# Performance work log

Measured on AMD Instinct MI355X. Metric: run time of the kernel, lower is better.

The kernel has to match this reference:

```python
import jax, jax.numpy as jnp
import numpy as np

EPS = 1e-6
H = 8          # num_heads
GAMMA = 0.99   # fixed decay (requires_grad=False in source)
RPE_LAYERS = 3


def srms(x):
    # SimpleRMSNorm: x / (rms(x) + eps), rms = ||x||_2 / sqrt(d) = sqrt(mean(x^2))
    return x / (jnp.sqrt(jnp.mean(x * x, axis=-1, keepdims=True)) + EPS)


def setup_inputs() -> dict:
    key = jax.random.key(0)
    B, N, E = 8, 2048, 512
    D1 = 1536            # int(3*512) // 8 * 8
    R = 512              # rpe_embedding
    ks = jax.random.split(key, 12)

    def lin(k, i, o):
        return jax.random.normal(k, (i, o), jnp.float32) * (i ** -0.5)

    x = jax.random.normal(ks[0], (B, N, E), jnp.float32)
    return {
        "x": x,
        "Wu": lin(ks[1], E, D1), "bu": jnp.zeros((D1,), jnp.float32),
        "Wv": lin(ks[2], E, D1), "bv": jnp.zeros((D1,), jnp.float32),
        "Wo": lin(ks[3], D1, E), "bo": jnp.zeros((E,), jnp.float32),
        "rpe_Win": lin(ks[4], 1, R), "rpe_bin": jnp.zeros((R,), jnp.float32),
        "rpe_W": jax.random.normal(ks[5], (RPE_LAYERS, R, R), jnp.float32) * (R ** -0.5),
        "rpe_b": jnp.zeros((RPE_LAYERS, R), jnp.float32),
        "rpe_Wout": lin(ks[6], R, D1), "rpe_bout": jnp.zeros((D1,), jnp.float32),
    }


def reference(x, Wu, bu, Wv, bv, Wo, bo, rpe_Win, rpe_bin, rpe_W, rpe_b, rpe_Wout, rpe_bout):
    B, N, E = x.shape
    u = jax.nn.silu(x @ Wu + bu)                     # b n d1
    v = jax.nn.silu(x @ Wv + bv)                     # b n d1
    D1 = v.shape[-1]
    D = D1 // H
    v = v.reshape(B, N, H, D).transpose(0, 2, 1, 3)  # b h n d

    # RPE MLP over positions: row 0 is the zero index, rows 1..N-1 are pos indices 1..N-1 (par_type=1)
    idx = jnp.arange(0, N, dtype=x.dtype)[:, None]   # (N, 1)
    h = idx @ rpe_Win + rpe_bin                      # (N, R)
    for i in range(RPE_LAYERS):                      # residual=False
        h = jax.nn.relu(srms(h)) @ rpe_W[i] + rpe_b[i]
    coeffs = jax.nn.relu(srms(h)) @ rpe_Wout + rpe_bout   # (N, H*D)
    coeffs = coeffs.reshape(N, H, D).transpose(1, 0, 2)   # h n d

    zero = coeffs[:, :1]                             # h 1 d  (a_0)
    pos = coeffs[:, 1:]                              # h n-1 d (a_1..a_{n-1})
    decay = GAMMA ** jnp.arange(1, N, dtype=x.dtype)[None, :, None]
    pos = pos * decay
    # causal: a = [a0, a1..a_{n-1}, a0]; act_type='none' -> identity
    a = jnp.concatenate([zero, pos, zero], axis=1)   # h, n+1, d

    # Toeplitz mixing via circular convolution of length 2n (torch.fft.rfft/irfft, norm='backward')
    m = 2 * N
    yf = jnp.fft.rfft(v, m, axis=2)                  # b h m/2+1 d (complex)
    af = jnp.fft.rfft(a, m, axis=1)[None]            # 1 h m/2+1 d
    out = jnp.fft.irfft(yf * af, m, axis=2)[:, :, :N, :]  # b h n d

    out = out.transpose(0, 2, 1, 3).reshape(B, N, D1)     # b n (h d)
    out = u * out
    return out @ Wo + bo
```

## Files before the change

### kernel.cpp

```cpp
#include <hip/hip_runtime.h>
#include <cstdint>


typedef unsigned short ushort_t;
typedef __attribute__((ext_vector_type(8))) short short8;
typedef __attribute__((ext_vector_type(4))) float f32x4;

#define AS1 __attribute__((address_space(1)))
#define AS3 __attribute__((address_space(3)))

#define SW1(j) ((j) ^ (((j) >> 4) & 15))
#define SW2(j) ((j) ^ ((((j) >> 6) & 7) << 1))

__device__ __forceinline__ int xcd_swz(int bid, int nwg) {
  return (bid & 7) * (nwg >> 3) + (bid >> 3);
}

__device__ __forceinline__ float bf2f(ushort_t b) {
  union { unsigned u; float f; } x; x.u = ((unsigned)b) << 16; return x.f;
}
__device__ __forceinline__ ushort_t f2bf(float f) {
  union { float f; unsigned u; } x; x.f = f;
  unsigned r = x.u + 0x7fffu + ((x.u >> 16) & 1u);
  return (ushort_t)(r >> 16);
}

__device__ __forceinline__ void gload_lds16(const void* g, void* l) {
  auto gp = reinterpret_cast<const AS1 unsigned*>(reinterpret_cast<uintptr_t>(g));
  auto lp = reinterpret_cast<AS3 unsigned*>(reinterpret_cast<uintptr_t>(l));
  __builtin_amdgcn_global_load_lds(gp, lp, 16, 0, 0);
}

template<int MODE>
__launch_bounds__(256, 2)
__global__ void gemm_bt(const ushort_t* __restrict__ A, const ushort_t* __restrict__ Bt,
                        const float* __restrict__ bias, void* __restrict__ Cout,
                        void* __restrict__ Cout2, int M, int N, int K, float lng)
{
  __shared__ ushort_t As[128 * 64];
  __shared__ ushort_t Bs[128 * 64];
  const int tid  = threadIdx.x;
  const int wave = tid >> 6, lane = tid & 63;
  const int nb = N >> 7;
  const int lbid = xcd_swz((int)blockIdx.x, (int)gridDim.x);
  const int bm = lbid / nb, bn = lbid % nb;
  const int m0 = bm << 7, n0 = bn << 7;
  const int lrow = lane & 15, quad = lane >> 4;
  const int wm = (wave >> 1) << 6, wn = (wave & 1) << 6;
  const int srow = lane >> 3;
  const int scol = (lane & 7) << 3;

  f32x4 acc[4][4] = {};

  for (int kt = 0; kt < K; kt += 64) {
    __syncthreads();
#pragma unroll
    for (int i = 0; i < 4; ++i) {
      const int ci  = i * 4 + wave;
      const int row = ci * 8 + srow;
      gload_lds16(A  + (long)(m0 + row) * K + kt + scol, (void*)&As[ci * 512]);
      gload_lds16(Bt + (long)(n0 + row) * K + kt + scol, (void*)&Bs[ci * 512]);
    }
    __syncthreads();
#pragma unroll
    for (int s = 0; s < 2; ++s) {
      short8 afr[4], bfr[4];
#pragma unroll
      for (int i = 0; i < 4; ++i)
        afr[i] = *(const short8*)&As[(wm + i * 16 + lrow) * 64 + s * 32 + quad * 8];
#pragma unroll
      for (int j = 0; j < 4; ++j)
        bfr[j] = *(const short8*)&Bs[(wn + j * 16 + lrow) * 64 + s * 32 + quad * 8];
#pragma unroll
      for (int i = 0; i < 4; ++i)
#pragma unroll
        for (int j = 0; j < 4; ++j)
          acc[i][j] = __builtin_amdgcn_mfma_f32_16x16x32_bf16(afr[i], bfr[j], acc[i][j], 0, 0, 0);
    }
  }

#pragma unroll
  for (int i = 0; i < 4; ++i) {
    const int rowb = m0 + wm + i * 16 + quad * 4;
#pragma unroll
    for (int j = 0; j < 4; ++j) {
      const int col = n0 + wn + j * 16 + lrow;
      const float bv = bias[col];
      if (MODE == 0) {
#pragma unroll
        for (int r = 0; r < 4; ++r)
          ((float*)Cout)[(long)(rowb + r) * N + col] = acc[i][j][r] + bv;
      } else {
        if (col < 1536) {
#pragma unroll
          for (int r = 0; r < 4; ++r) {
            float val = acc[i][j][r] + bv;
            float sv = val / (1.f + __expf(-val));
            ((ushort_t*)Cout)[(long)(rowb + r) * 1536 + col] = f2bf(sv);
          }
        } else {
          union { ushort_t h[4]; uint2 u2; } pk;
#pragma unroll
          for (int r = 0; r < 4; ++r) {
            float val = acc[i][j][r] + bv;
            float sv = val / (1.f + __expf(-val));
            pk.h[r] = f2bf(sv);
          }
          *(uint2*)((ushort_t*)Cout2 + (long)(col - 1536) * 16384 + rowb) = pk.u2;
        }
      }
    }
  }
}

template<int MODE>
__launch_bounds__(256, 2)
__global__ void gemm64_bt(const ushort_t* __restrict__ A, const float* __restrict__ Af,
                          const ushort_t* __restrict__ Bt,
                          const float* __restrict__ bias, float* __restrict__ Cout,
                          int M, int N, int K, float lng)
{
  constexpr bool NORM = (MODE >= 4);
  __shared__ ushort_t As[64 * 64];
  __shared__ ushort_t Bs[64 * 64];
  __shared__ float rsc[64];
  const int tid = threadIdx.x, wave = tid >> 6, lane = tid & 63;
  const int nb = N >> 6;
  const int lbid = xcd_swz((int)blockIdx.x, (int)gridDim.x);
  const int bm = lbid / nb, bn = lbid % nb;
  const int m0 = bm << 6, n0 = bn << 6;
  const int lrow = lane & 15, quad = lane >> 4;
  const int wm = (wave >> 1) << 5, wn = (wave & 1) << 5;
  const int srow = lane >> 3, scol = (lane & 7) << 3;

  if (NORM) {
    const int prow = tid >> 2, pq = tid & 3;
    const float* hr = Af + (long)(m0 + prow) * 512 + pq * 128;
    float ss = 0.f;
#pragma unroll 8
    for (int c = 0; c < 128; c += 4) {
      float4 f = *(const float4*)(hr + c);
      ss += f.x * f.x + f.y * f.y + f.z * f.z + f.w * f.w;
    }
    ss += __shfl_xor(ss, 1);
    ss += __shfl_xor(ss, 2);
    if (pq == 0) rsc[prow] = 1.f / (sqrtf(ss * (1.f / 512.f)) + 1e-6f);
  }

  f32x4 acc[2][2] = {};

  for (int kt = 0; kt < K; kt += 64) {
    __syncthreads();
#pragma unroll
    for (int i = 0; i < 2; ++i) {
      const int ci = i * 4 + wave;
      const int row = ci * 8 + srow;
      if (!NORM) {
        gload_lds16(A + (long)(m0 + row) * K + kt + scol, (void*)&As[ci * 512]);
      } else {
        const float* hp = Af + (long)(m0 + row) * 512 + kt + scol;
        float4 f0 = *(const float4*)hp;
        float4 f1 = *(const float4*)(hp + 4);
        const float sc = rsc[row];
        unsigned p0 = (unsigned)f2bf(fmaxf(f0.x * sc, 0.f)) |
                      ((unsigned)f2bf(fmaxf(f0.y * sc, 0.f)) << 16);
        unsigned p1 = (unsigned)f2bf(fmaxf(f0.z * sc, 0.f)) |
                      ((unsigned)f2bf(fmaxf(f0.w * sc, 0.f)) << 16);
        unsigned p2 = (unsigned)f2bf(fmaxf(f1.x * sc, 0.f)) |
                      ((unsigned)f2bf(fmaxf(f1.y * sc, 0.f)) << 16);
        unsigned p3 = (unsigned)f2bf(fmaxf(f1.z * sc, 0.f)) |
                      ((unsigned)f2bf(fmaxf(f1.w * sc, 0.f)) << 16);
        *(uint4*)&As[ci * 512 + srow * 64 + scol] = make_uint4(p0, p1, p2, p3);
      }
      gload_lds16(Bt + (long)(n0 + row) * K + kt + scol, (void*)&Bs[ci * 512]);
    }
    __syncthreads();
#pragma unroll
    for (int s = 0; s < 2; ++s) {
      short8 afr[2], bfr[2];
#pragma unroll
      for (int i = 0; i < 2; ++i)
        afr[i] = *(const short8*)&As[(wm + i * 16 + lrow) * 64 + s * 32 + quad * 8];
#pragma unroll
      for (int j = 0; j < 2; ++j)
        bfr[j] = *(const short8*)&Bs[(wn + j * 16 + lrow) * 64 + s * 32 + quad * 8];
#pragma unroll
      for (int i = 0; i < 2; ++i)
#pragma unroll
        for (int j = 0; j < 2; ++j)
          acc[i][j] = __builtin_amdgcn_mfma_f32_16x16x32_bf16(afr[i], bfr[j], acc[i][j], 0, 0, 0);
    }
  }

#pragma unroll
  for (int i = 0; i < 2; ++i) {
    const int rowb = m0 + wm + i * 16 + quad * 4;
#pragma unroll
    for (int j = 0; j < 2; ++j) {
      const int col = n0 + wn + j * 16 + lrow;
      const float bv = bias[col];
#pragma unroll
      for (int r = 0; r < 4; ++r) {
        const int row = rowb + r;
        float val = acc[i][j][r] + bv;
        if (MODE == 0 || MODE == 4) Cout[(long)row * N + col] = val;
        else                        Cout[(long)col * M + row] = val * __expf(lng * (float)row);
      }
    }
  }
}

__device__ __forceinline__ void srms_relu_store(float v0, float v1, ushort_t* out,
                                                long rowbase, int tid)
{
  float ss = v0 * v0 + v1 * v1;
#pragma unroll
  for (int off = 32; off; off >>= 1) ss += __shfl_down(ss, off);
  __shared__ float ps[4];
  const int wave = tid >> 6, lane = tid & 63;
  if (lane == 0) ps[wave] = ss;
  __syncthreads();
  float tot = ps[0] + ps[1] + ps[2] + ps[3];
  float sc = 1.f / (sqrtf(tot * (1.f / 512.f)) + 1e-6f);
  out[rowbase + tid]       = f2bf(fmaxf(v0 * sc, 0.f));
  out[rowbase + tid + 256] = f2bf(fmaxf(v1 * sc, 0.f));
}

__device__ __forceinline__ void wtrans_body(const float* __restrict__ src,
                                            ushort_t* __restrict__ dst,
                                            int K, int N, int lb, int tid,
                                            float (*tile)[33])
{
  const int nbx = N >> 5;
  const int bx = lb % nbx, by = lb / nbx;
  const int n0 = bx << 5, k0 = by << 5;
  const int tx = tid & 31, ty = tid >> 5;
  for (int yy = ty; yy < 32; yy += 8)
    tile[yy][tx] = src[(long)(k0 + yy) * N + n0 + tx];
  __syncthreads();
  for (int yy = ty; yy < 32; yy += 8)
    dst[(long)(n0 + yy) * K + k0 + tx] = f2bf(tile[tx][yy]);
}

__launch_bounds__(256)
__global__ void prep_all(const float* __restrict__ Wu, const float* __restrict__ Wv,
                         const float* __restrict__ Wo, const float* __restrict__ rW,
                         const float* __restrict__ rWout,
                         const float* __restrict__ bu, const float* __restrict__ bv,
                         const float* __restrict__ x,
                         const float* __restrict__ rWin, const float* __restrict__ rbin,
                         ushort_t* __restrict__ wuvt, ushort_t* __restrict__ wot,
                         ushort_t* __restrict__ wrt, ushort_t* __restrict__ wroutt,
                         float* __restrict__ buvb, ushort_t* __restrict__ xb,
                         float2* __restrict__ twg, float2* __restrict__ twh,
                         ushort_t* __restrict__ a0)
{
  __shared__ float tile[32][33];
  const int bid = blockIdx.x, tid = threadIdx.x;
  if (bid < 3840) {
    const float* src; ushort_t* dst; int K, N, lb;
    if (bid < 768)       { src = Wu;    dst = wuvt;              K = 512;  N = 1536; lb = bid; }
    else if (bid < 1536) { src = Wv;    dst = wuvt + 1536L*512;  K = 512;  N = 1536; lb = bid - 768; }
    else if (bid < 2304) { src = Wo;    dst = wot;               K = 1536; N = 512;  lb = bid - 1536; }
    else if (bid < 2560) { src = rW;              dst = wrt;              K = 512; N = 512; lb = bid - 2304; }
    else if (bid < 2816) { src = rW + 512L*512;   dst = wrt + 512L*512;   K = 512; N = 512; lb = bid - 2560; }
    else if (bid < 3072) { src = rW + 2L*512*512; dst = wrt + 2L*512*512; K = 512; N = 512; lb = bid - 2816; }
    else                 { src = rWout; dst = wroutt;            K = 512;  N = 1536; lb = bid - 3072; }
    wtrans_body(src, dst, K, N, lb, tid, tile);
  } else if (bid < 3846) {
    int i = (bid - 3840) * 256 + tid;
    if (i < 1536) { buvb[i] = bu[i]; buvb[1536 + i] = bv[i]; }
  } else if (bid < 12038) {
    long i = (long)(bid - 3846) * 1024 + tid * 4;
    float4 f = *(const float4*)(x + i);
    unsigned lo = (unsigned)f2bf(f.x) | ((unsigned)f2bf(f.y) << 16);
    unsigned hi = (unsigned)f2bf(f.z) | ((unsigned)f2bf(f.w) << 16);
    *(uint2*)(xb + i) = make_uint2(lo, hi);
  } else if (bid < 12046) {
    int j = (bid - 12038) * 256 + tid;
    float s, c;
    __sincosf((float)j * (6.283185307179586f / 2048.f), &s, &c);
    twg[j] = make_float2(c, -s);
    float s2, c2;
    __sincosf((float)j * (3.14159265358979f / 2048.f), &s2, &c2);
    twh[j] = make_float2(c2, -s2);
  } else {
    const int n = bid - 12046;
    const float fn = (float)n;
    float v0 = fn * rWin[tid] + rbin[tid];
    float v1 = fn * rWin[tid + 256] + rbin[tid + 256];
    srms_relu_store(v0, v1, a0, (long)n * 512, tid);
  }
}

__device__ __forceinline__ float2 cmulf(float2 a, float2 b) {
  return make_float2(a.x * b.x - a.y * b.y, a.x * b.y + a.y * b.x);
}
__device__ __forceinline__ float4 c2add(float4 p, float4 q){
  return make_float4(p.x+q.x, p.y+q.y, p.z+q.z, p.w+q.w);
}
__device__ __forceinline__ float4 c2sub(float4 p, float4 q){
  return make_float4(p.x-q.x, p.y-q.y, p.z-q.z, p.w-q.w);
}
__device__ __forceinline__ float4 c2mni(float4 z){
  return make_float4(z.y, -z.x, z.w, -z.z);
}
__device__ __forceinline__ float4 c2w8(float4 z){
  const float s = 0.70710678118654752f;
  return make_float4(s*(z.x+z.y), s*(z.y-z.x), s*(z.z+z.w), s*(z.w-z.z));
}
__device__ __forceinline__ float4 c2w83(float4 z){
  const float s = 0.70710678118654752f;
  return make_float4(s*(z.y-z.x), -s*(z.x+z.y), s*(z.w-z.z), -s*(z.z+z.w));
}
__device__ __forceinline__ float4 c2mul(float4 z, float2 w){
  return make_float4(z.x*w.x - z.y*w.y, z.x*w.y + z.y*w.x,
                     z.z*w.x - z.w*w.y, z.z*w.y + z.w*w.x);
}

__device__ __forceinline__ void dft8d(const float4* u, float4* y)
{
  float4 a0=c2add(u[0],u[4]), a1=c2add(u[1],u[5]), a2=c2add(u[2],u[6]), a3=c2add(u[3],u[7]);
  float4 b0=c2sub(u[0],u[4]), b1=c2w8(c2sub(u[1],u[5])), b2=c2mni(c2sub(u[2],u[6])), b3=c2w83(c2sub(u[3],u[7]));
  float4 c0=c2add(a0,a2), c1=c2sub(a0,a2), c2=c2add(a1,a3), c3=c2mni(c2sub(a1,a3));
  y[0]=c2add(c0,c2); y[2]=c2add(c1,c3); y[4]=c2sub(c0,c2); y[6]=c2sub(c1,c3);
  float4 d0=c2add(b0,b2), d1=c2sub(b0,b2), d2=c2add(b1,b3), d3=c2mni(c2sub(b1,b3));
  y[1]=c2add(d0,d2); y[3]=c2add(d1,d3); y[5]=c2sub(d0,d2); y[7]=c2sub(d1,d3);
}
__device__ __forceinline__ void dft8d_hz(const float4* u, float4* y)
{
  float4 b1=c2w8(u[1]), b2=c2mni(u[2]), b3=c2w83(u[3]);
  float4 c0=c2add(u[0],u[2]), c1=c2sub(u[0],u[2]), c2=c2add(u[1],u[3]), c3=c2mni(c2sub(u[1],u[3]));
  y[0]=c2add(c0,c2); y[2]=c2add(c1,c3); y[4]=c2sub(c0,c2); y[6]=c2sub(c1,c3);
  float4 d0=c2add(u[0],b2), d1=c2sub(u[0],b2), d2=c2add(b1,b3), d3=c2mni(c2sub(b1,b3));
  y[1]=c2add(d0,d2); y[3]=c2add(d1,d3); y[5]=c2sub(d0,d2); y[7]=c2sub(d1,d3);
}

template<bool HZ>
__device__ void fft2048_ip4(float4* b, const float2* __restrict__ tw, int tid)
{
  float4 u[8], y[8];
  {
    const int i = tid;
#pragma unroll
    for (int m = 0; m < (HZ ? 4 : 8); ++m) u[m] = b[i + 256*m];
    if (HZ) dft8d_hz(u, y); else dft8d(u, y);
    __syncthreads();
    const int j = i << 3;
#pragma unroll
    for (int m = 0; m < 8; ++m) b[SW1(j + m)] = y[m];
  }
  __syncthreads();
  {
    const int i = tid, k = i & 7, tb = k << 5;
    float2 w[8];
#pragma unroll
    for (int m = 1; m < 8; ++m) w[m] = tw[m * tb];
#pragma unroll
    for (int m = 0; m < 8; ++m) u[m] = b[SW1(i + 256*m)];
#pragma unroll
    for (int m = 1; m < 8; ++m) u[m] = c2mul(u[m], w[m]);
    dft8d(u, y);
    __syncthreads();
    const int j = ((i - k) << 3) + k;
#pragma unroll
    for (int m = 0; m < 8; ++m) b[SW2(j + 8*m)] = y[m];
  }
  __syncthreads();
  {
    const int i = tid, k = i & 63, tb = k << 2;
    float2 w[8];
#pragma unroll
    for (int m = 1; m < 8; ++m) w[m] = tw[m * tb];
#pragma unroll
    for (int m = 0; m < 8; ++m) u[m] = b[SW2(i + 256*m)];
#pragma unroll
    for (int m = 1; m < 8; ++m) u[m] = c2mul(u[m], w[m]);
    dft8d(u, y);
    __syncthreads();
    const int j = ((i - k) << 3) + k;
#pragma unroll
    for (int m = 0; m < 8; ++m) b[j + 64*m] = y[m];
  }
  __syncthreads();
#pragma unroll
  for (int hh = 0; hh < 2; ++hh) {
    const int i = tid + (hh << 8);
    float2 w1 = tw[i], w2 = tw[2 * i], w3 = tw[3 * i];
    float4 q0 = b[i], q1 = b[i + 512], q2 = b[i + 1024], q3 = b[i + 1536];
    q1 = c2mul(q1, w1); q2 = c2mul(q2, w2); q3 = c2mul(q3, w3);
    float4 v0 = c2add(q0, q2), v2 = c2sub(q0, q2);
    float4 v1 = c2add(q1, q3), v3 = c2mni(c2sub(q1, q3));
    b[i]        = c2add(v0, v1);
    b[i + 512]  = c2add(v2, v3);
    b[i + 1024] = c2sub(v0, v1);
    b[i + 1536] = c2sub(v2, v3);
  }
  __syncthreads();
}

__launch_bounds__(256, 4)
__global__ void fft_kernel_spec(const float* __restrict__ kern, float2* __restrict__ af,
                                const float2* __restrict__ twg, const float2* __restrict__ twh)
{
  __shared__ float4 bx[2048];
  const int tid = threadIdx.x;
  const int c0 = (int)blockIdx.x * 2;
  const float* ka = kern + (long)c0 * 2048;
  const float* kb = ka + 2048;
  for (int j = tid; j < 1024; j += 256) {
    float2 A = *(const float2*)(ka + 2 * j);
    float2 B = *(const float2*)(kb + 2 * j);
    bx[j] = make_float4(A.x, A.y, B.x, B.y);
  }
  __syncthreads();
  fft2048_ip4<true>(bx, twg, tid);
  float2* af0 = af + (long)c0 * 2052;
  float2* af1 = af0 + 2052;
  for (int k = tid; k <= 1024; k += 256) {
    const float2 W = twh[k];
    const int kn = (2048 - k) & 2047;
    const float4 Zk4 = bx[k], Zn4 = bx[kn];
    {
      float2 Zk = make_float2(Zk4.x, Zk4.y), Zn = make_float2(Zn4.x, Zn4.y);
      float2 E = make_float2(0.5f * (Zk.x + Zn.x), 0.5f * (Zk.y - Zn.y));
      float2 O = make_float2(0.5f * (Zk.y + Zn.y), 0.5f * (Zn.x - Zk.x));
      float2 WO = cmulf(W, O);
      af0[k] = make_float2(E.x + WO.x, E.y + WO.y);
      if (k != 0 && k != 1024) af0[2048 - k] = make_float2(E.x - WO.x, -(E.y - WO.y));
      if (k == 0)              af0[2048]     = make_float2(E.x - WO.x, -(E.y - WO.y));
    }
    {
      float2 Zk = make_float2(Zk4.z, Zk4.w), Zn = make_float2(Zn4.z, Zn4.w);
      float2 E = make_float2(0.5f * (Zk.x + Zn.x), 0.5f * (Zk.y - Zn.y));
      float2 O = make_float2(0.5f * (Zk.y + Zn.y), 0.5f * (Zn.x - Zk.x));
      float2 WO = cmulf(W, O);
      af1[k] = make_float2(E.x + WO.x, E.y + WO.y);
      if (k != 0 && k != 1024) af1[2048 - k] = make_float2(E.x - WO.x, -(E.y - WO.y));
      if (k == 0)              af1[2048]     = make_float2(E.x - WO.x, -(E.y - WO.y));
    }
  }
}

__launch_bounds__(256, 4)
__global__ void fft_conv(ushort_t* __restrict__ vt, const float2* __restrict__ af,
                         const float2* __restrict__ twg, const float2* __restrict__ twh)
{
  __shared__ float4 bx[2048];
  const int tid = threadIdx.x;
  const long s0 = (long)blockIdx.x * 2;
  const int c = (int)(s0 >> 3);
  ushort_t* vsa = vt + s0 * 2048;
  ushort_t* vsb = vsa + 2048;
#pragma unroll
  for (int jj = 0; jj < 4; ++jj) {
    const int j = tid + jj * 256;
    unsigned pa = *(const unsigned*)(vsa + 2 * j);
    unsigned pb = *(const unsigned*)(vsb + 2 * j);
    bx[j] = make_float4(bf2f((ushort_t)(pa & 0xffffu)), bf2f((ushort_t)(pa >> 16)),
                        bf2f((ushort_t)(pb & 0xffffu)), bf2f((ushort_t)(pb >> 16)));
  }
  __syncthreads();
  fft2048_ip4<true>(bx, twg, tid);
  const float2* afc = af + (long)c * 2052;
  for (int k = tid; k <= 1024; k += 256) {
    const float2 A0 = afc[k], A1 = afc[2048 - k], W = twh[k];
    const float2 cW = make_float2(W.x, -W.y);
    const int kn = (2048 - k) & 2047;
    const float4 Zk4 = bx[k], Zn4 = bx[kn];
    float2 ya0, yn0, ya1, yn1;
    {
      float2 Zk = make_float2(Zk4.x, Zk4.y), Zn = make_float2(Zn4.x, Zn4.y);
      float2 E = make_float2(0.5f * (Zk.x + Zn.x), 0.5f * (Zk.y - Zn.y));
      float2 O = make_float2(0.5f * (Zk.y + Zn.y), 0.5f * (Zn.x - Zk.x));
      float2 WO = cmulf(W, O);
      float2 Xk = make_float2(E.x + WO.x, E.y + WO.y);
      float2 Xn = make_float2(E.x - WO.x, -(E.y - WO.y));
      float2 Pk = cmulf(Xk, A0);
      float2 Pn = cmulf(Xn, A1);
      float2 E2 = make_float2(0.5f * (Pk.x + Pn.x), 0.5f * (Pk.y - Pn.y));
      float2 G  = make_float2(0.5f * (Pk.x - Pn.x), 0.5f * (Pk.y + Pn.y));
      float2 Fo = cmulf(cW, G);
      ya0 = make_float2(E2.x - Fo.y, -(E2.y + Fo.x));
      yn0 = make_float2(E2.x + Fo.y, E2.y - Fo.x);
    }
    {
      float2 Zk = make_float2(Zk4.z, Zk4.w), Zn = make_float2(Zn4.z, Zn4.w);
      float2 E = make_float2(0.5f * (Zk.x + Zn.x), 0.5f * (Zk.y - Zn.y));
      float2 O = make_float2(0.5f * (Zk.y + Zn.y), 0.5f * (Zn.x - Zk.x));
      float2 WO = cmulf(W, O);
      float2 Xk = make_float2(E.x + WO.x, E.y + WO.y);
      float2 Xn = make_float2(E.x - WO.x, -(E.y - WO.y));
      float2 Pk = cmulf(Xk, A0);
      float2 Pn = cmulf(Xn, A1);
      float2 E2 = make_float2(0.5f * (Pk.x + Pn.x), 0.5f * (Pk.y - Pn.y));
      float2 G  = make_float2(0.5f * (Pk.x - Pn.x), 0.5f * (Pk.y + Pn.y));
      float2 Fo = cmulf(cW, G);
      ya1 = make_float2(E2.x - Fo.y, -(E2.y + Fo.x));
      yn1 = make_float2(E2.x + Fo.y, E2.y - Fo.x);
    }
    bx[k] = make_float4(ya0.x, ya0.y, ya1.x, ya1.y);
    if (k != 0 && k != 1024)
      bx[2048 - k] = make_float4(yn0.x, yn0.y, yn1.x, yn1.y);
  }
  __syncthreads();
  fft2048_ip4<false>(bx, twg, tid);
  const float inv = 1.f / 2048.f;
#pragma unroll
  for (int jj = 0; jj < 4; ++jj) {
    const int j = tid + jj * 256;
    float4 r = bx[j];
    unsigned oa = (unsigned)f2bf(r.x * inv) | ((unsigned)f2bf(-r.y * inv) << 16);
    unsigned ob = (unsigned)f2bf(r.z * inv) | ((unsigned)f2bf(-r.w * inv) << 16);
    *(unsigned*)(vsa + 2 * j) = oa;
    *(unsigned*)(vsb + 2 * j) = ob;
  }
}

__launch_bounds__(256)
__global__ void gate_trans(const ushort_t* __restrict__ convt, ushort_t* __restrict__ u)
{
  __shared__ ushort_t tile[64][65];
  const int bc = (int)blockIdx.x % 24, br = (int)blockIdx.x / 24;
  const int c0 = bc << 6, r0 = br << 6;
  const int tx = threadIdx.x & 63, ty = threadIdx.x >> 6;
  for (int yy = ty; yy < 64; yy += 4)
    tile[yy][tx] = convt[(long)(c0 + yy) * 16384 + r0 + tx];
  __syncthreads();
  for (int yy = ty; yy < 64; yy += 4) {
    long ui = (long)(r0 + yy) * 1536 + c0 + tx;
    float uu = bf2f(u[ui]);
    float cc = bf2f(tile[tx][yy]);
    u[ui] = f2bf(uu * cc);
  }
}

extern "C" void kernel_launch(void* const* d_in, const int* in_sizes, int n_in,
                              void* d_out, int out_size, void* d_ws, size_t ws_size,
                              hipStream_t stream)
{
  const float* x     = (const float*)d_in[0];
  const float* Wu    = (const float*)d_in[1];
  const float* bu    = (const float*)d_in[2];
  const float* Wv    = (const float*)d_in[3];
  const float* bv    = (const float*)d_in[4];
  const float* Wo    = (const float*)d_in[5];
  const float* bo    = (const float*)d_in[6];
  const float* rWin  = (const float*)d_in[7];
  const float* rbin  = (const float*)d_in[8];
  const float* rW    = (const float*)d_in[9];
  const float* rb    = (const float*)d_in[10];
  const float* rWout = (const float*)d_in[11];
  const float* rbout = (const float*)d_in[12];

  char* base = (char*)d_ws;
  size_t off = 0;
  auto alloc = [&](size_t bytes) -> char* {
    size_t r = (off + 255) & ~(size_t)255; off = r + bytes; return base + r;
  };
  ushort_t* wuvt   = (ushort_t*)alloc(3072L * 512 * 2);
  ushort_t* wot    = (ushort_t*)alloc(512L * 1536 * 2);
  ushort_t* wrt    = (ushort_t*)alloc(3L * 512 * 512 * 2);
  ushort_t* wroutt = (ushort_t*)alloc(1536L * 512 * 2);
  float*    buvb   = (float*)   alloc(3072L * 4);
  ushort_t* a0     = (ushort_t*)alloc(2048L * 512 * 2);
  float2*   af     = (float2*)  alloc(1536L * 2052 * 8);
  float2*   twg    = (float2*)  alloc(2048L * 8);
  float2*   twh    = (float2*)  alloc(2048L * 8);
  char*     X      = alloc(16384L * 512 * 2);
  ushort_t* u      = (ushort_t*)alloc(16384L * 1536 * 2);
  ushort_t* vt     = (ushort_t*)alloc(1536L * 16384 * 2);
  ushort_t* xb   = (ushort_t*)X;
  float*    hA   = (float*)X;
  float*    hB   = (float*)(X + 4L * 1024 * 1024);
  float*    kern = (float*)(X + 4L * 1024 * 1024);

  const float lng = -0.01005033585350145f;

  prep_all<<<dim3(14094), dim3(256), 0, stream>>>(
      Wu, Wv, Wo, rW, rWout, bu, bv, x, rWin, rbin,
      wuvt, wot, wrt, wroutt, buvb, xb, twg, twh, a0);

  gemm_bt<3><<<dim3(3072), dim3(256), 0, stream>>>(xb, wuvt, buvb, u, vt,
                                                   16384, 3072, 512, 0.f);

  gemm64_bt<0><<<dim3(256), dim3(256), 0, stream>>>(a0, nullptr, wrt,
                                                    rb, hA, 2048, 512, 512, 0.f);
  gemm64_bt<4><<<dim3(256), dim3(256), 0, stream>>>(nullptr, hA, wrt + 512L*512,
                                                    rb + 512, hB, 2048, 512, 512, 0.f);
  gemm64_bt<4><<<dim3(256), dim3(256), 0, stream>>>(nullptr, hB, wrt + 2L*512*512,
                                                    rb + 1024, hA, 2048, 512, 512, 0.f);
  gemm64_bt<5><<<dim3(768), dim3(256), 0, stream>>>(nullptr, hA, wroutt,
                                                    rbout, kern, 2048, 1536, 512, lng);
  fft_kernel_spec<<<dim3(768), dim3(256), 0, stream>>>(kern, af, twg, twh);

  fft_conv<<<dim3(6144), dim3(256), 0, stream>>>(vt, af, twg, twh);
  gate_trans<<<dim3(6144), dim3(256), 0, stream>>>(vt, u);
  gemm_bt<0><<<dim3(512), dim3(256), 0, stream>>>(u, wot, bo, d_out, nullptr,
                                                  16384, 512, 1536, 0.f);
}
```

Baseline: 459.7 us.

## Replace packed 2048-point real-FFT trick with full 4096-point complex FFT

The FFT convolution previously packed two real channels into one complex 2048-point transform, then split them with a half-length twiddle and post-processing step. It now runs a full 4096-point complex FFT with two real channels packed as real and imaginary parts. The kernel spectrum is stored at full length, and the inverse transform uses a conjugate trick. This removes the split/merge post-processing and one twiddle table. In exchange it roughly doubles the FFT work and LDS traffic per block and doubles the spectrum buffer size.

```diff
diff --git a/kernel.cpp b/kernel.cpp
--- a/kernel.cpp
+++ b/kernel.cpp
@@ -9,8 +9,8 @@
 #define AS1 __attribute__((address_space(1)))
 #define AS3 __attribute__((address_space(3)))
 
-#define SW1(j) ((j) ^ (((j) >> 4) & 15))
-#define SW2(j) ((j) ^ ((((j) >> 6) & 7) << 1))
+#define SWA(j) ((j) ^ (((j) >> 3) & 15))
+#define SWB(j) ((j) ^ ((((j) >> 6) & 7) << 1))
 
 __device__ __forceinline__ int xcd_swz(int bid, int nwg) {
   return (bid & 7) * (nwg >> 3) + (bid >> 3);
@@ -252,8 +252,7 @@
                          ushort_t* __restrict__ wuvt, ushort_t* __restrict__ wot,
                          ushort_t* __restrict__ wrt, ushort_t* __restrict__ wroutt,
                          float* __restrict__ buvb, ushort_t* __restrict__ xb,
-                         float2* __restrict__ twg, float2* __restrict__ twh,
-                         ushort_t* __restrict__ a0)
+                         float2* __restrict__ twf, ushort_t* __restrict__ a0)
 {
   __shared__ float tile[32][33];
   const int bid = blockIdx.x, tid = threadIdx.x;
@@ -276,16 +275,13 @@
     unsigned lo = (unsigned)f2bf(f.x) | ((unsigned)f2bf(f.y) << 16);
     unsigned hi = (unsigned)f2bf(f.z) | ((unsigned)f2bf(f.w) << 16);
     *(uint2*)(xb + i) = make_uint2(lo, hi);
-  } else if (bid < 12046) {
+  } else if (bid < 12054) {
     int j = (bid - 12038) * 256 + tid;
     float s, c;
-    __sincosf((float)j * (6.283185307179586f / 2048.f), &s, &c);
-    twg[j] = make_float2(c, -s);
-    float s2, c2;
-    __sincosf((float)j * (3.14159265358979f / 2048.f), &s2, &c2);
-    twh[j] = make_float2(c2, -s2);
+    __sincosf((float)j * (6.283185307179586f / 4096.f), &s, &c);
+    twf[j] = make_float2(c, -s);
   } else {
-    const int n = bid - 12046;
+    const int n = bid - 12054;
     const float fn = (float)n;
     float v0 = fn * rWin[tid] + rbin[tid];
     float v1 = fn * rWin[tid + 256] + rbin[tid + 256];
@@ -296,157 +292,159 @@
 __device__ __forceinline__ float2 cmulf(float2 a, float2 b) {
   return make_float2(a.x * b.x - a.y * b.y, a.x * b.y + a.y * b.x);
 }
-__device__ __forceinline__ float4 c2add(float4 p, float4 q){
-  return make_float4(p.x+q.x, p.y+q.y, p.z+q.z, p.w+q.w);
-}
-__device__ __forceinline__ float4 c2sub(float4 p, float4 q){
-  return make_float4(p.x-q.x, p.y-q.y, p.z-q.z, p.w-q.w);
-}
-__device__ __forceinline__ float4 c2mni(float4 z){
-  return make_float4(z.y, -z.x, z.w, -z.z);
-}
-__device__ __forceinline__ float4 c2w8(float4 z){
+__device__ __forceinline__ float2 cadds(float2 a, float2 b){ return make_float2(a.x+b.x, a.y+b.y); }
+__device__ __forceinline__ float2 csubs(float2 a, float2 b){ return make_float2(a.x-b.x, a.y-b.y); }
+__device__ __forceinline__ float2 cmnis(float2 z){ return make_float2(z.y, -z.x); }
+__device__ __forceinline__ float2 cw8s(float2 z){
   const float s = 0.70710678118654752f;
-  return make_float4(s*(z.x+z.y), s*(z.y-z.x), s*(z.z+z.w), s*(z.w-z.z));
-}
-__device__ __forceinline__ float4 c2w83(float4 z){
+  return make_float2(s*(z.x+z.y), s*(z.y-z.x));
+}
+__device__ __forceinline__ float2 cw83s(float2 z){
   const float s = 0.70710678118654752f;
-  return make_float4(s*(z.y-z.x), -s*(z.x+z.y), s*(z.w-z.z), -s*(z.z+z.w));
-}
-__device__ __forceinline__ float4 c2mul(float4 z, float2 w){
-  return make_float4(z.x*w.x - z.y*w.y, z.x*w.y + z.y*w.x,
-                     z.z*w.x - z.w*w.y, z.z*w.y + z.w*w.x);
-}
-
-__device__ __forceinline__ void dft8d(const float4* u, float4* y)
-{
-  float4 a0=c2add(u[0],u[4]), a1=c2add(u[1],u[5]), a2=c2add(u[2],u[6]), a3=c2add(u[3],u[7]);
-  float4 b0=c2sub(u[0],u[4]), b1=c2w8(c2sub(u[1],u[5])), b2=c2mni(c2sub(u[2],u[6])), b3=c2w83(c2sub(u[3],u[7]));
-  float4 c0=c2add(a0,a2), c1=c2sub(a0,a2), c2=c2add(a1,a3), c3=c2mni(c2sub(a1,a3));
-  y[0]=c2add(c0,c2); y[2]=c2add(c1,c3); y[4]=c2sub(c0,c2); y[6]=c2sub(c1,c3);
-  float4 d0=c2add(b0,b2), d1=c2sub(b0,b2), d2=c2add(b1,b3), d3=c2mni(c2sub(b1,b3));
-  y[1]=c2add(d0,d2); y[3]=c2add(d1,d3); y[5]=c2sub(d0,d2); y[7]=c2sub(d1,d3);
-}
-__device__ __forceinline__ void dft8d_hz(const float4* u, float4* y)
-{
-  float4 b1=c2w8(u[1]), b2=c2mni(u[2]), b3=c2w83(u[3]);
-  float4 c0=c2add(u[0],u[2]), c1=c2sub(u[0],u[2]), c2=c2add(u[1],u[3]), c3=c2mni(c2sub(u[1],u[3]));
-  y[0]=c2add(c0,c2); y[2]=c2add(c1,c3); y[4]=c2sub(c0,c2); y[6]=c2sub(c1,c3);
-  float4 d0=c2add(u[0],b2), d1=c2sub(u[0],b2), d2=c2add(b1,b3), d3=c2mni(c2sub(b1,b3));
-  y[1]=c2add(d0,d2); y[3]=c2add(d1,d3); y[5]=c2sub(d0,d2); y[7]=c2sub(d1,d3);
+  return make_float2(s*(z.y-z.x), -s*(z.x+z.y));
+}
+
+__device__ __forceinline__ void dft8s(const float2* u, float2* y)
+{
+  float2 a0=cadds(u[0],u[4]), a1=cadds(u[1],u[5]), a2=cadds(u[2],u[6]), a3=cadds(u[3],u[7]);
+  float2 b0=csubs(u[0],u[4]), b1=cw8s(csubs(u[1],u[5])), b2=cmnis(csubs(u[2],u[6])), b3=cw83s(csubs(u[3],u[7]));
+  float2 c0=cadds(a0,a2), c1=csubs(a0,a2), c2=cadds(a1,a3), c3=cmnis(csubs(a1,a3));
+  y[0]=cadds(c0,c2); y[2]=cadds(c1,c3); y[4]=csubs(c0,c2); y[6]=csubs(c1,c3);
+  float2 d0=cadds(b0,b2), d1=csubs(b0,b2), d2=cadds(b1,b3), d3=cmnis(csubs(b1,b3));
+  y[1]=cadds(d0,d2); y[3]=cadds(d1,d3); y[5]=csubs(d0,d2); y[7]=csubs(d1,d3);
+}
+__device__ __forceinline__ void dft8s_hz(const float2* u, float2* y)
+{
+  float2 b1=cw8s(u[1]), b2=cmnis(u[2]), b3=cw83s(u[3]);
+  float2 c0=cadds(u[0],u[2]), c1=csubs(u[0],u[2]), c2=cadds(u[1],u[3]), c3=cmnis(csubs(u[1],u[3]));
+  y[0]=cadds(c0,c2); y[2]=cadds(c1,c3); y[4]=csubs(c0,c2); y[6]=csubs(c1,c3);
+  float2 d0=cadds(u[0],b2), d1=csubs(u[0],b2), d2=cadds(b1,b3), d3=cmnis(csubs(b1,b3));
+  y[1]=cadds(d0,d2); y[3]=cadds(d1,d3); y[5]=csubs(d0,d2); y[7]=csubs(d1,d3);
 }
 
 template<bool HZ>
-__device__ void fft2048_ip4(float4* b, const float2* __restrict__ tw, int tid)
-{
-  float4 u[8], y[8];
-  {
-    const int i = tid;
-#pragma unroll
-    for (int m = 0; m < (HZ ? 4 : 8); ++m) u[m] = b[i + 256*m];
-    if (HZ) dft8d_hz(u, y); else dft8d(u, y);
-    __syncthreads();
-    const int j = i << 3;
-#pragma unroll
-    for (int m = 0; m < 8; ++m) b[SW1(j + m)] = y[m];
-  }
-  __syncthreads();
-  {
-    const int i = tid, k = i & 7, tb = k << 5;
-    float2 w[8];
-#pragma unroll
-    for (int m = 1; m < 8; ++m) w[m] = tw[m * tb];
-#pragma unroll
-    for (int m = 0; m < 8; ++m) u[m] = b[SW1(i + 256*m)];
-#pragma unroll
-    for (int m = 1; m < 8; ++m) u[m] = c2mul(u[m], w[m]);
-    dft8d(u, y);
-    __syncthreads();
-    const int j = ((i - k) << 3) + k;
-#pragma unroll
-    for (int m = 0; m < 8; ++m) b[SW2(j + 8*m)] = y[m];
-  }
-  __syncthreads();
-  {
-    const int i = tid, k = i & 63, tb = k << 2;
-    float2 w[8];
-#pragma unroll
-    for (int m = 1; m < 8; ++m) w[m] = tw[m * tb];
-#pragma unroll
-    for (int m = 0; m < 8; ++m) u[m] = b[SW2(i + 256*m)];
-#pragma unroll
-    for (int m = 1; m < 8; ++m) u[m] = c2mul(u[m], w[m]);
-    dft8d(u, y);
-    __syncthreads();
-    const int j = ((i - k) << 3) + k;
-#pragma unroll
-    for (int m = 0; m < 8; ++m) b[j + 64*m] = y[m];
-  }
-  __syncthreads();
-#pragma unroll
-  for (int hh = 0; hh < 2; ++hh) {
-    const int i = tid + (hh << 8);
-    float2 w1 = tw[i], w2 = tw[2 * i], w3 = tw[3 * i];
-    float4 q0 = b[i], q1 = b[i + 512], q2 = b[i + 1024], q3 = b[i + 1536];
-    q1 = c2mul(q1, w1); q2 = c2mul(q2, w2); q3 = c2mul(q3, w3);
-    float4 v0 = c2add(q0, q2), v2 = c2sub(q0, q2);
-    float4 v1 = c2add(q1, q3), v3 = c2mni(c2sub(q1, q3));
-    b[i]        = c2add(v0, v1);
-    b[i + 512]  = c2add(v2, v3);
-    b[i + 1024] = c2sub(v0, v1);
-    b[i + 1536] = c2sub(v2, v3);
-  }
-  __syncthreads();
+__device__ __forceinline__ void f4k_s1(float2* b, int tid)
+{
+  float2 u[8], u2[8], y[8], y2[8];
+#pragma unroll
+  for (int m = 0; m < (HZ ? 4 : 8); ++m) {
+    u[m]  = b[tid + 512*m];
+    u2[m] = b[tid + 256 + 512*m];
+  }
+  if (HZ) { dft8s_hz(u, y); dft8s_hz(u2, y2); }
+  else    { dft8s(u, y);    dft8s(u2, y2); }
+  __syncthreads();
+  const int j1 = tid << 3;
+#pragma unroll
+  for (int m = 0; m < 8; ++m) {
+    b[SWA(j1 + m)]        = y[m];
+    b[SWA(j1 + 2048 + m)] = y2[m];
+  }
+}
+
+__device__ __forceinline__ void f4k_s2(float2* b, const float2* __restrict__ tw, int tid)
+{
+  const int k = tid & 7;
+  float2 w[8];
+#pragma unroll
+  for (int m = 1; m < 8; ++m) w[m] = tw[m * k * 64];
+  float2 u[8], u2[8], y[8], y2[8];
+#pragma unroll
+  for (int m = 0; m < 8; ++m) {
+    u[m]  = b[SWA(tid + 512*m)];
+    u2[m] = b[SWA(tid + 256 + 512*m)];
+  }
+#pragma unroll
+  for (int m = 1; m < 8; ++m) { u[m] = cmulf(u[m], w[m]); u2[m] = cmulf(u2[m], w[m]); }
+  dft8s(u, y); dft8s(u2, y2);
+  __syncthreads();
+  const int j1 = ((tid - k) << 3) + k;
+#pragma unroll
+  for (int m = 0; m < 8; ++m) {
+    b[SWB(j1 + 8*m)]        = y[m];
+    b[SWB(j1 + 2048 + 8*m)] = y2[m];
+  }
+}
+
+__device__ __forceinline__ void f4k_s3(float2* b, const float2* __restrict__ tw, int tid)
+{
+  const int k = tid & 63;
+  float2 w[8];
+#pragma unroll
+  for (int m = 1; m < 8; ++m) w[m] = tw[m * k * 8];
+  float2 u[8], u2[8], y[8], y2[8];
+#pragma unroll
+  for (int m = 0; m < 8; ++m) {
+    u[m]  = b[SWB(tid + 512*m)];
+    u2[m] = b[SWB(tid + 256 + 512*m)];
+  }
+#pragma unroll
+  for (int m = 1; m < 8; ++m) { u[m] = cmulf(u[m], w[m]); u2[m] = cmulf(u2[m], w[m]); }
+  dft8s(u, y); dft8s(u2, y2);
+  __syncthreads();
+  const int j1 = ((tid - k) << 3) + k;
+#pragma unroll
+  for (int m = 0; m < 8; ++m) {
+    b[j1 + 64*m]        = y[m];
+    b[j1 + 2048 + 64*m] = y2[m];
+  }
 }
 
 __launch_bounds__(256, 4)
 __global__ void fft_kernel_spec(const float* __restrict__ kern, float2* __restrict__ af,
-                                const float2* __restrict__ twg, const float2* __restrict__ twh)
-{
-  __shared__ float4 bx[2048];
+                                const float2* __restrict__ twf)
+{
+  __shared__ float2 b[4096];
   const int tid = threadIdx.x;
   const int c0 = (int)blockIdx.x * 2;
   const float* ka = kern + (long)c0 * 2048;
   const float* kb = ka + 2048;
-  for (int j = tid; j < 1024; j += 256) {
-    float2 A = *(const float2*)(ka + 2 * j);
-    float2 B = *(const float2*)(kb + 2 * j);
-    bx[j] = make_float4(A.x, A.y, B.x, B.y);
-  }
-  __syncthreads();
-  fft2048_ip4<true>(bx, twg, tid);
-  float2* af0 = af + (long)c0 * 2052;
-  float2* af1 = af0 + 2052;
-  for (int k = tid; k <= 1024; k += 256) {
-    const float2 W = twh[k];
-    const int kn = (2048 - k) & 2047;
-    const float4 Zk4 = bx[k], Zn4 = bx[kn];
-    {
-      float2 Zk = make_float2(Zk4.x, Zk4.y), Zn = make_float2(Zn4.x, Zn4.y);
-      float2 E = make_float2(0.5f * (Zk.x + Zn.x), 0.5f * (Zk.y - Zn.y));
-      float2 O = make_float2(0.5f * (Zk.y + Zn.y), 0.5f * (Zn.x - Zk.x));
-      float2 WO = cmulf(W, O);
-      af0[k] = make_float2(E.x + WO.x, E.y + WO.y);
-      if (k != 0 && k != 1024) af0[2048 - k] = make_float2(E.x - WO.x, -(E.y - WO.y));
-      if (k == 0)              af0[2048]     = make_float2(E.x - WO.x, -(E.y - WO.y));
-    }
-    {
-      float2 Zk = make_float2(Zk4.z, Zk4.w), Zn = make_float2(Zn4.z, Zn4.w);
-      float2 E = make_float2(0.5f * (Zk.x + Zn.x), 0.5f * (Zk.y - Zn.y));
-      float2 O = make_float2(0.5f * (Zk.y + Zn.y), 0.5f * (Zn.x - Zk.x));
-      float2 WO = cmulf(W, O);
-      af1[k] = make_float2(E.x + WO.x, E.y + WO.y);
-      if (k != 0 && k != 1024) af1[2048 - k] = make_float2(E.x - WO.x, -(E.y - WO.y));
-      if (k == 0)              af1[2048]     = make_float2(E.x - WO.x, -(E.y - WO.y));
+#pragma unroll
+  for (int jj = 0; jj < 8; ++jj) {
+    const int n = tid + jj * 256;
+    b[n] = make_float2(ka[n], kb[n]);
+  }
+  __syncthreads();
+  f4k_s1<true>(b, twf ? tid : tid);
+  __syncthreads();
+  f4k_s2(b, twf, tid);
+  __syncthreads();
+  f4k_s3(b, twf, tid);
+  __syncthreads();
+#pragma unroll
+  for (int h = 0; h < 2; ++h) {
+    const int i = tid + (h << 8);
+    float2 u[8], y[8];
+#pragma unroll
+    for (int m = 0; m < 8; ++m) u[m] = b[i + 512*m];
+#pragma unroll
+    for (int m = 1; m < 8; ++m) u[m] = cmulf(u[m], twf[m * i]);
+    dft8s(u, y);
+#pragma unroll
+    for (int m = 0; m < 8; ++m) b[i + 512*m] = y[m];
+  }
+  __syncthreads();
+  float2* af0 = af + (long)c0 * 4096;
+  float2* af1 = af0 + 4096;
+#pragma unroll
+  for (int h = 0; h < 2; ++h) {
+    const int i = tid + (h << 8);
+#pragma unroll
+    for (int m = 0; m < 8; ++m) {
+      const int k = i + 512*m;
+      const int kn = (4096 - k) & 4095;
+      const float2 Zk = b[k], Zn = b[kn];
+      af0[k] = make_float2(0.5f * (Zk.x + Zn.x), 0.5f * (Zk.y - Zn.y));
+      af1[k] = make_float2(0.5f * (Zk.y + Zn.y), 0.5f * (Zn.x - Zk.x));
     }
   }
 }
 
 __launch_bounds__(256, 4)
 __global__ void fft_conv(ushort_t* __restrict__ vt, const float2* __restrict__ af,
-                         const float2* __restrict__ twg, const float2* __restrict__ twh)
-{
-  __shared__ float4 bx[2048];
+                         const float2* __restrict__ twf)
+{
+  __shared__ float2 b[4096];
   const int tid = threadIdx.x;
   const long s0 = (long)blockIdx.x * 2;
   const int c = (int)(s0 >> 3);
@@ -457,63 +455,57 @@
     const int j = tid + jj * 256;
     unsigned pa = *(const unsigned*)(vsa + 2 * j);
     unsigned pb = *(const unsigned*)(vsb + 2 * j);
-    bx[j] = make_float4(bf2f((ushort_t)(pa & 0xffffu)), bf2f((ushort_t)(pa >> 16)),
-                        bf2f((ushort_t)(pb & 0xffffu)), bf2f((ushort_t)(pb >> 16)));
-  }
-  __syncthreads();
-  fft2048_ip4<true>(bx, twg, tid);
-  const float2* afc = af + (long)c * 2052;
-  for (int k = tid; k <= 1024; k += 256) {
-    const float2 A0 = afc[k], A1 = afc[2048 - k], W = twh[k];
-    const float2 cW = make_float2(W.x, -W.y);
-    const int kn = (2048 - k) & 2047;
-    const float4 Zk4 = bx[k], Zn4 = bx[kn];
-    float2 ya0, yn0, ya1, yn1;
-    {
-      float2 Zk = make_float2(Zk4.x, Zk4.y), Zn = make_float2(Zn4.x, Zn4.y);
-      float2 E = make_float2(0.5f * (Zk.x + Zn.x), 0.5f * (Zk.y - Zn.y));
-      float2 O = make_float2(0.5f * (Zk.y + Zn.y), 0.5f * (Zn.x - Zk.x));
-      float2 WO = cmulf(W, O);
-      float2 Xk = make_float2(E.x + WO.x, E.y + WO.y);
-      float2 Xn = make_float2(E.x - WO.x, -(E.y - WO.y));
-      float2 Pk = cmulf(Xk, A0);
-      float2 Pn = cmulf(Xn, A1);
-      float2 E2 = make_float2(0.5f * (Pk.x + Pn.x), 0.5f * (Pk.y - Pn.y));
-      float2 G  = make_float2(0.5f * (Pk.x - Pn.x), 0.5f * (Pk.y + Pn.y));
-      float2 Fo = cmulf(cW, G);
-      ya0 = make_float2(E2.x - Fo.y, -(E2.y + Fo.x));
-      yn0 = make_float2(E2.x + Fo.y, E2.y - Fo.x);
-    }
-    {
-      float2 Zk = make_float2(Zk4.z, Zk4.w), Zn = make_float2(Zn4.z, Zn4.w);
-      float2 E = make_float2(0.5f * (Zk.x + Zn.x), 0.5f * (Zk.y - Zn.y));
-      float2 O = make_float2(0.5f * (Zk.y + Zn.y), 0.5f * (Zn.x - Zk.x));
-      float2 WO = cmulf(W, O);
-      float2 Xk = make_float2(E.x + WO.x, E.y + WO.y);
-      float2 Xn = make_float2(E.x - WO.x, -(E.y - WO.y));
-      float2 Pk = cmulf(Xk, A0);
-      float2 Pn = cmulf(Xn, A1);
-      float2 E2 = make_float2(0.5f * (Pk.x + Pn.x), 0.5f * (Pk.y - Pn.y));
-      float2 G  = make_float2(0.5f * (Pk.x - Pn.x), 0.5f * (Pk.y + Pn.y));
-      float2 Fo = cmulf(cW, G);
-      ya1 = make_float2(E2.x - Fo.y, -(E2.y + Fo.x));
-      yn1 = make_float2(E2.x + Fo.y, E2.y - Fo.x);
-    }
-    bx[k] = make_float4(ya0.x, ya0.y, ya1.x, ya1.y);
-    if (k != 0 && k != 1024)
-      bx[2048 - k] = make_float4(yn0.x, yn0.y, yn1.x, yn1.y);
-  }
-  __syncthreads();
-  fft2048_ip4<false>(bx, twg, tid);
-  const float inv = 1.f / 2048.f;
-#pragma unroll
-  for (int jj = 0; jj < 4; ++jj) {
-    const int j = tid + jj * 256;
-    float4 r = bx[j];
-    unsigned oa = (unsigned)f2bf(r.x * inv) | ((unsigned)f2bf(-r.y * inv) << 16);
-    unsigned ob = (unsigned)f2bf(r.z * inv) | ((unsigned)f2bf(-r.w * inv) << 16);
-    *(unsigned*)(vsa + 2 * j) = oa;
-    *(unsigned*)(vsb + 2 * j) = ob;
+    float4 z2 = make_float4(bf2f((ushort_t)(pa & 0xffffu)), bf2f((ushort_t)(pb & 0xffffu)),
+                            bf2f((ushort_t)(pa >> 16)),     bf2f((ushort_t)(pb >> 16)));
+    *(float4*)&b[2 * j] = z2;
+  }
+  __syncthreads();
+  f4k_s1<true>(b, tid);
+  __syncthreads();
+  f4k_s2(b, twf, tid);
+  __syncthreads();
+  f4k_s3(b, twf, tid);
+  __syncthreads();
+  const float2* afc = af + (long)c * 4096;
+#pragma unroll
+  for (int h = 0; h < 2; ++h) {
+    const int i = tid + (h << 8);
+    float2 u[8], y[8];
+#pragma unroll
+    for (int m = 0; m < 8; ++m) u[m] = b[i + 512*m];
+#pragma unroll
+    for (int m = 1; m < 8; ++m) u[m] = cmulf(u[m], twf[m * i]);
+    dft8s(u, y);
+#pragma unroll
+    for (int m = 0; m < 8; ++m) {
+      const float2 A = afc[i + 512*m];
+      const float2 Y = cmulf(y[m], A);
+      b[i + 512*m] = make_float2(Y.x, -Y.y);
+    }
+  }
+  __syncthreads();
+  f4k_s1<false>(b, tid);
+  __syncthreads();
+  f4k_s2(b, twf, tid);
+  __syncthreads();
+  f4k_s3(b, twf, tid);
+  __syncthreads();
+  const float inv = 1.f / 4096.f;
+#pragma unroll
+  for (int h = 0; h < 2; ++h) {
+    const int i = tid + (h << 8);
+    float2 u[8], y[8];
+#pragma unroll
+    for (int m = 0; m < 8; ++m) u[m] = b[i + 512*m];
+#pragma unroll
+    for (int m = 1; m < 8; ++m) u[m] = cmulf(u[m], twf[m * i]);
+    dft8s(u, y);
+#pragma unroll
+    for (int m = 0; m < 4; ++m) {
+      const int n = i + 512*m;
+      vsa[n] = f2bf(y[m].x * inv);
+      vsb[n] = f2bf(-y[m].y * inv);
+    }
   }
 }
 
@@ -564,9 +556,8 @@
   ushort_t* wroutt = (ushort_t*)alloc(1536L * 512 * 2);
   float*    buvb   = (float*)   alloc(3072L * 4);
   ushort_t* a0     = (ushort_t*)alloc(2048L * 512 * 2);
-  float2*   af     = (float2*)  alloc(1536L * 2052 * 8);
-  float2*   twg    = (float2*)  alloc(2048L * 8);
-  float2*   twh    = (float2*)  alloc(2048L * 8);
+  float2*   af     = (float2*)  alloc(1536L * 4096 * 8);
+  float2*   twf    = (float2*)  alloc(4096L * 8);
   char*     X      = alloc(16384L * 512 * 2);
   ushort_t* u      = (ushort_t*)alloc(16384L * 1536 * 2);
   ushort_t* vt     = (ushort_t*)alloc(1536L * 16384 * 2);
@@ -577,9 +568,9 @@
 
   const float lng = -0.01005033585350145f;
 
-  prep_all<<<dim3(14094), dim3(256), 0, stream>>>(
+  prep_all<<<dim3(14102), dim3(256), 0, stream>>>(
       Wu, Wv, Wo, rW, rWout, bu, bv, x, rWin, rbin,
-      wuvt, wot, wrt, wroutt, buvb, xb, twg, twh, a0);
+      wuvt, wot, wrt, wroutt, buvb, xb, twf, a0);
 
   gemm_bt<3><<<dim3(3072), dim3(256), 0, stream>>>(xb, wuvt, buvb, u, vt,
                                                    16384, 3072, 512, 0.f);
@@ -592,9 +583,9 @@
                                                     rb + 1024, hA, 2048, 512, 512, 0.f);
   gemm64_bt<5><<<dim3(768), dim3(256), 0, stream>>>(nullptr, hA, wroutt,
                                                     rbout, kern, 2048, 1536, 512, lng);
-  fft_kernel_spec<<<dim3(768), dim3(256), 0, stream>>>(kern, af, twg, twh);
-
-  fft_conv<<<dim3(6144), dim3(256), 0, stream>>>(vt, af, twg, twh);
+  fft_kernel_spec<<<dim3(768), dim3(256), 0, stream>>>(kern, af, twf);
+
+  fft_conv<<<dim3(6144), dim3(256), 0, stream>>>(vt, af, twf);
   gate_trans<<<dim3(6144), dim3(256), 0, stream>>>(vt, u);
   gemm_bt<0><<<dim3(512), dim3(256), 0, stream>>>(u, wot, bo, d_out, nullptr,
                                                   16384, 512, 1536, 0.f);
```

After: 596.6 us. 29.8% more time.
